# Kernel tuning notes

Hardware: AMD Instinct MI355X
Metric: run time of the kernel (lower is better)

The kernel has to match this reference:

```python
import jax, jax.numpy as jnp
import numpy as np

Q_MAX = 127.0  # int8 symmetric quant range
EPS = 1e-7

def setup_inputs() -> dict:
    key = jax.random.key(0)
    k1, k2, k3, k4 = jax.random.split(key, 4)
    M, K, N = 8192, 4096, 4096
    x = jax.random.normal(k1, (M, K), dtype=jnp.float32)
    # int8 weight stored as int32 for portability; values in [-127, 127]
    weight_i8 = jax.random.randint(k2, (N, K), -127, 128, dtype=jnp.int32)
    # per-output-channel weight scale (small positive)
    w_scale = jax.random.uniform(k3, (N,), dtype=jnp.float32) * 0.01 + 1e-4
    bias = jax.random.normal(k4, (N,), dtype=jnp.float32)
    return {"x": x, "weight_i8": weight_i8, "w_scale": w_scale, "bias": bias}

def reference(x, weight_i8, w_scale, bias):
    # per-token dynamic symmetric quantization of activations
    absmax = jnp.max(jnp.abs(x), axis=-1, keepdims=True)            # [M, 1]
    x_scale = jnp.maximum(absmax, EPS) / Q_MAX                       # [M, 1]
    x_q = jnp.clip(jnp.round(x / x_scale), -Q_MAX, Q_MAX)            # [M, K] int values in fp32
    acc = jnp.einsum('mk,nk->mn', x_q, weight_i8.astype(jnp.float32))  # [M, N]
    out = acc * x_scale * w_scale[None, :] + bias[None, :]
    return out
```

## Files before the change

### kernel.cpp

```cpp
#include <hip/hip_runtime.h>
#include <stdint.h>

#define Q_MAX_F 127.0f
#define EPS_F 1e-7f

typedef int   v4i  __attribute__((ext_vector_type(4)));
typedef int   v16i __attribute__((ext_vector_type(16)));
typedef float v4f  __attribute__((ext_vector_type(4)));

__global__ __launch_bounds__(256) void prep_kernel(
    const float* __restrict__ x, int8_t* __restrict__ xq,
    float* __restrict__ xscale,
    const int* __restrict__ w, int8_t* __restrict__ wq,
    int M, int K, long n4, int QB) {
  const int t = threadIdx.x;
  if ((int)blockIdx.x < QB) {
    __shared__ float sm[4];
    for (int row = blockIdx.x; row < M; row += QB) {
      const float* xr = x + (size_t)row * K + t * 16;
      float v[16];
      float m = 0.f;
#pragma unroll
      for (int c = 0; c < 4; ++c) {
        v4f f = *(const v4f*)(xr + c * 4);
#pragma unroll
        for (int j = 0; j < 4; ++j) {
          v[c * 4 + j] = f[j];
          m = fmaxf(m, fabsf(f[j]));
        }
      }
#pragma unroll
      for (int off = 32; off; off >>= 1) m = fmaxf(m, __shfl_xor(m, off));
      if ((t & 63) == 0) sm[t >> 6] = m;
      __syncthreads();
      m = fmaxf(fmaxf(sm[0], sm[1]), fmaxf(sm[2], sm[3]));
      __syncthreads();
      const float s = fmaxf(m, EPS_F) / Q_MAX_F;
      const float inv = 1.0f / s;
      if (t == 0) xscale[row] = s;
      v4i pk;
#pragma unroll
      for (int c = 0; c < 4; ++c) {
        int pw = 0;
#pragma unroll
        for (int j = 0; j < 4; ++j) {
          float q = rintf(v[c * 4 + j] * inv);
          q = fminf(fmaxf(q, -127.f), 127.f);
          pw |= ((int)q & 0xff) << (8 * j);
        }
        pk[c] = pw;
      }
      *(v4i*)(xq + (size_t)row * K + t * 16) = pk;
    }
  } else {
    const long stride = (long)(gridDim.x - QB) * 256;
    for (long i = (long)((int)blockIdx.x - QB) * 256 + t; i < n4; i += stride) {
      v4i a = ((const v4i*)w)[i];
      ((int*)wq)[i] = (a[0] & 0xff) | ((a[1] & 0xff) << 8) |
                      ((a[2] & 0xff) << 16) | ((a[3] & 0xff) << 24);
    }
  }
}

#define BM 256
#define BN 256

__global__ __launch_bounds__(512, 2) void w8a8_gemm_kernel(
    const int8_t* __restrict__ xq, const int8_t* __restrict__ wq,
    const float* __restrict__ xscale, const float* __restrict__ wscale,
    const float* __restrict__ bias, float* __restrict__ out,
    int M, int N, int K) {
  extern __shared__ char lds[];

  const int t = threadIdx.x;
  const int lane = t & 63;
  const int wid = t >> 6;
  const int wr = wid >> 2;
  const int wc = wid & 3;

  const int nwg = gridDim.x;
  int bid = blockIdx.x;
  int wg = ((nwg & 7) == 0) ? ((bid & 7) * (nwg >> 3) + (bid >> 3)) : bid;

  const int nbn = N / BN;
  const int bm = (wg / nbn) * BM;
  const int bn = (wg % nbn) * BN;

  const char* gA = (const char*)xq + (size_t)bm * K;
  const char* gB = (const char*)wq + (size_t)bn * K;

  v16i acc[4][2] = {};

  auto stage_part = [&](int kt, int p) {
    const char* gsrc = p ? gB : gA;
    char* dstbase = lds + (size_t)(kt & 3) * 32768 + p * 16384;
#pragma unroll
    for (int i = 0; i < 2; ++i) {
      const int lin = i * 8192 + wid * 1024 + lane * 16;
      const int row = lin >> 6;
      const int cs = (lane & 3) ^ ((row >> 1) & 3);
      const char* src = gsrc + (size_t)row * K + kt * 64 + cs * 16;
      __builtin_amdgcn_global_load_lds(
          (const __attribute__((address_space(1))) void*)src,
          (__attribute__((address_space(3))) void*)(dstbase + i * 8192 + wid * 1024),
          16, 0, 0);
    }
  };

  const int NT = K / 64;
  const int cl = lane & 31;
  const int ch = lane >> 5;

  for (int kt = 0; kt < 3; ++kt) { stage_part(kt, 0); stage_part(kt, 1); }
  asm volatile("s_waitcnt vmcnt(8)" ::: "memory");
  asm volatile("s_barrier" ::: "memory");

  for (int kt = 0; kt < NT; ++kt) {
    const char* bufA = lds + (size_t)(kt & 3) * 32768;
    const char* bufB = bufA + 16384;

    if (kt + 3 < NT) { stage_part(kt + 3, 0); stage_part(kt + 3, 1); }

    v4i a[2][4], b[2][2];
#pragma unroll
    for (int ks = 0; ks < 2; ++ks) {
#pragma unroll
      for (int fi = 0; fi < 4; ++fi) {
        const int r = wr * 128 + fi * 32 + cl;
        const int c = (ch + 2 * ks) ^ ((r >> 1) & 3);
        a[ks][fi] = *(const v4i*)(bufA + r * 64 + (c << 4));
      }
#pragma unroll
      for (int fj = 0; fj < 2; ++fj) {
        const int r = wc * 64 + fj * 32 + cl;
        const int c = (ch + 2 * ks) ^ ((r >> 1) & 3);
        b[ks][fj] = *(const v4i*)(bufB + r * 64 + (c << 4));
      }
    }

    __builtin_amdgcn_s_setprio(1);
#pragma unroll
    for (int ks = 0; ks < 2; ++ks)
#pragma unroll
      for (int fi = 0; fi < 4; ++fi)
#pragma unroll
        for (int fj = 0; fj < 2; ++fj)
          acc[fi][fj] = __builtin_amdgcn_mfma_i32_32x32x32_i8(
              a[ks][fi], b[ks][fj], acc[fi][fj], 0, 0, 0);
    __builtin_amdgcn_s_setprio(0);

    if (kt <= NT - 4)      asm volatile("s_waitcnt vmcnt(8)" ::: "memory");
    else if (kt == NT - 3) asm volatile("s_waitcnt vmcnt(4)" ::: "memory");
    else if (kt == NT - 2) asm volatile("s_waitcnt vmcnt(0)" ::: "memory");
    asm volatile("s_barrier" ::: "memory");
  }

  const int hl = lane >> 5;
  const float wsc0 = wscale[bn + wc * 64 + cl];
  const float wsc1 = wscale[bn + wc * 64 + 32 + cl];
  const float bs0 = bias[bn + wc * 64 + cl];
  const float bs1 = bias[bn + wc * 64 + 32 + cl];
#pragma unroll
  for (int fi = 0; fi < 4; ++fi) {
#pragma unroll
    for (int r = 0; r < 16; ++r) {
      const int grow = bm + wr * 128 + fi * 32 + (r & 3) + 8 * (r >> 2) + 4 * hl;
      const float xs = xscale[grow];
      float* orow = out + (size_t)grow * N + bn + wc * 64 + cl;
      orow[0]  = (float)acc[fi][0][r] * (xs * wsc0) + bs0;
      orow[32] = (float)acc[fi][1][r] * (xs * wsc1) + bs1;
    }
  }
}

extern "C" void kernel_launch(void* const* d_in, const int* in_sizes, int n_in,
                              void* d_out, int out_size, void* d_ws, size_t ws_size,
                              hipStream_t stream) {
  const float* x = (const float*)d_in[0];
  const int* w = (const int*)d_in[1];
  const float* wscale = (const float*)d_in[2];
  const float* bias = (const float*)d_in[3];
  float* out = (float*)d_out;

  const int N = in_sizes[2];
  const long wk = (long)in_sizes[1];
  const int K = (int)(wk / N);
  const int M = (int)((long)in_sizes[0] / K);

  int8_t* xq = (int8_t*)d_ws;
  int8_t* wq = xq + (size_t)M * K;
  float* xscale = (float*)(wq + (size_t)N * K);

  const long n4 = (long)N * K / 4;
  const int QB = 2048, PB = 2048;
  prep_kernel<<<QB + PB, 256, 0, stream>>>(x, xq, xscale, w, wq, M, K, n4, QB);

  const int nwg = (M / BM) * (N / BN);
  w8a8_gemm_kernel<<<nwg, 512, 131072, stream>>>(xq, wq, xscale, wscale, bias,
                                                 out, M, N, K);
}
```

Measured before the change: 415.2 us.

## Pre-pack operands in MFMA fragment order and load A directly to registers

The quantize and weight-pack kernels now write int8 data in a fragment-major layout that matches the MFMA operand order, so each lane's 16-byte fragment sits contiguous in global memory. The GEMM now loads A fragments straight from global into double-buffered registers, one tile ahead, and stages only B through LDS. This cuts the LDS footprint from 128KB of dynamic to 64KB of static and removes A's LDS traffic and swizzle math. In exchange, A's global loads are exposed to latency with only one stage of prefetch, and prep is split into two separate launches.

Result: slower. 458.2 us (+10.4%).

```diff
diff --git a/kernel.cpp b/kernel.cpp
--- a/kernel.cpp
+++ b/kernel.cpp
@@ -8,69 +8,91 @@
 typedef int   v16i __attribute__((ext_vector_type(16)));
 typedef float v4f  __attribute__((ext_vector_type(4)));
 
-__global__ __launch_bounds__(256) void prep_kernel(
+
+__global__ __launch_bounds__(256) void quant_x_kernel(
     const float* __restrict__ x, int8_t* __restrict__ xq,
-    float* __restrict__ xscale,
-    const int* __restrict__ w, int8_t* __restrict__ wq,
-    int M, int K, long n4, int QB) {
+    float* __restrict__ xscale, int M, int K, int QB) {
   const int t = threadIdx.x;
-  if ((int)blockIdx.x < QB) {
-    __shared__ float sm[4];
-    for (int row = blockIdx.x; row < M; row += QB) {
-      const float* xr = x + (size_t)row * K + t * 16;
-      float v[16];
-      float m = 0.f;
-#pragma unroll
-      for (int c = 0; c < 4; ++c) {
-        v4f f = *(const v4f*)(xr + c * 4);
-#pragma unroll
-        for (int j = 0; j < 4; ++j) {
-          v[c * 4 + j] = f[j];
-          m = fmaxf(m, fabsf(f[j]));
-        }
+  const int KT = K >> 6;
+  __shared__ float sm[4];
+  for (int row = blockIdx.x; row < M; row += QB) {
+    const float* xr = x + (size_t)row * K + t * 16;
+    float v[16];
+    float m = 0.f;
+#pragma unroll
+    for (int c = 0; c < 4; ++c) {
+      v4f f = *(const v4f*)(xr + c * 4);
+#pragma unroll
+      for (int j = 0; j < 4; ++j) {
+        v[c * 4 + j] = f[j];
+        m = fmaxf(m, fabsf(f[j]));
       }
-#pragma unroll
-      for (int off = 32; off; off >>= 1) m = fmaxf(m, __shfl_xor(m, off));
-      if ((t & 63) == 0) sm[t >> 6] = m;
-      __syncthreads();
-      m = fmaxf(fmaxf(sm[0], sm[1]), fmaxf(sm[2], sm[3]));
-      __syncthreads();
-      const float s = fmaxf(m, EPS_F) / Q_MAX_F;
-      const float inv = 1.0f / s;
-      if (t == 0) xscale[row] = s;
-      v4i pk;
-#pragma unroll
-      for (int c = 0; c < 4; ++c) {
-        int pw = 0;
-#pragma unroll
-        for (int j = 0; j < 4; ++j) {
-          float q = rintf(v[c * 4 + j] * inv);
-          q = fminf(fmaxf(q, -127.f), 127.f);
-          pw |= ((int)q & 0xff) << (8 * j);
-        }
-        pk[c] = pw;
+    }
+#pragma unroll
+    for (int off = 32; off; off >>= 1) m = fmaxf(m, __shfl_xor(m, off));
+    if ((t & 63) == 0) sm[t >> 6] = m;
+    __syncthreads();
+    m = fmaxf(fmaxf(sm[0], sm[1]), fmaxf(sm[2], sm[3]));
+    __syncthreads();
+    const float s = fmaxf(m, EPS_F) / Q_MAX_F;
+    const float inv = 1.0f / s;
+    if (t == 0) xscale[row] = s;
+    v4i pk;
+#pragma unroll
+    for (int c = 0; c < 4; ++c) {
+      int pw = 0;
+#pragma unroll
+      for (int j = 0; j < 4; ++j) {
+        float q = rintf(v[c * 4 + j] * inv);
+        q = fminf(fmaxf(q, -127.f), 127.f);
+        pw |= ((int)q & 0xff) << (8 * j);
       }
-      *(v4i*)(xq + (size_t)row * K + t * 16) = pk;
-    }
-  } else {
-    const long stride = (long)(gridDim.x - QB) * 256;
-    for (long i = (long)((int)blockIdx.x - QB) * 256 + t; i < n4; i += stride) {
-      v4i a = ((const v4i*)w)[i];
-      ((int*)wq)[i] = (a[0] & 0xff) | ((a[1] & 0xff) << 8) |
-                      ((a[2] & 0xff) << 16) | ((a[3] & 0xff) << 24);
-    }
-  }
-}
-
-#define BM 256
-#define BN 256
+      pk[c] = pw;
+    }
+    const int rb = row >> 7, f2 = (row >> 5) & 3, cl = row & 31;
+    const int kt = t >> 2, ks = (t >> 1) & 1, ch = t & 1;
+    const size_t flat =
+        ((((size_t)rb * KT + kt) * 2 + ks) * 4 + f2) * 64 + ch * 32 + cl;
+    *(v4i*)(xq + flat * 16) = pk;
+  }
+}
+
+__global__ __launch_bounds__(256) void pack_w_kernel(
+    const int* __restrict__ w, int8_t* __restrict__ wq, int K, long nchunks) {
+  const int KT = K >> 6;
+  const long stride = (long)gridDim.x * 256;
+  for (long o = (long)blockIdx.x * 256 + threadIdx.x; o < nchunks;
+       o += stride) {
+    const int cl = (int)(o & 31);
+    const int ch = (int)((o >> 5) & 1);
+    const int fj = (int)((o >> 6) & 1);
+    const int ks = (int)((o >> 7) & 1);
+    const long rest = o >> 8;
+    const int kt = (int)(rest & (KT - 1));
+    const long cb = rest >> 6;
+    const long n = cb * 64 + fj * 32 + cl;
+    const long k16 = (long)kt * 4 + ks * 2 + ch;
+    const int* src = w + n * K + k16 * 16;
+    v4i outw;
+#pragma unroll
+    for (int c = 0; c < 4; ++c) {
+      v4i a = *(const v4i*)(src + c * 4);
+      outw[c] = (a[0] & 0xff) | ((a[1] & 0xff) << 8) |
+                ((a[2] & 0xff) << 16) | ((a[3] & 0xff) << 24);
+    }
+    *(v4i*)(wq + o * 16) = outw;
+  }
+}
+
+#define BMg 256
+#define BNg 256
 
 __global__ __launch_bounds__(512, 2) void w8a8_gemm_kernel(
     const int8_t* __restrict__ xq, const int8_t* __restrict__ wq,
     const float* __restrict__ xscale, const float* __restrict__ wscale,
     const float* __restrict__ bias, float* __restrict__ out,
     int M, int N, int K) {
-  extern __shared__ char lds[];
+  __shared__ __align__(16) char lds[65536];
 
   const int t = threadIdx.x;
   const int lane = t & 63;
@@ -82,62 +104,53 @@
   int bid = blockIdx.x;
   int wg = ((nwg & 7) == 0) ? ((bid & 7) * (nwg >> 3) + (bid >> 3)) : bid;
 
-  const int nbn = N / BN;
-  const int bm = (wg / nbn) * BM;
-  const int bn = (wg % nbn) * BN;
-
-  const char* gA = (const char*)xq + (size_t)bm * K;
-  const char* gB = (const char*)wq + (size_t)bn * K;
+  const int nbn = N / BNg;
+  const int bm = (wg / nbn) * BMg;
+  const int bn = (wg % nbn) * BNg;
+
+  const int KT = K >> 6;
+  const int NT = KT;
+
+  const char* aBase = (const char*)xq +
+                      ((size_t)((bm >> 7) + wr) * KT) * 8192 +
+                      (size_t)lane * 16;
+  const char* bBase = (const char*)wq + ((size_t)(bn >> 6) * KT) * 4096;
 
   v16i acc[4][2] = {};
-
-  auto stage_part = [&](int kt, int p) {
-    const char* gsrc = p ? gB : gA;
-    char* dstbase = lds + (size_t)(kt & 3) * 32768 + p * 16384;
+  v4i aA[2][4], aB[2][4];
+
+  auto loadA = [&](v4i (*dst)[4], int kt) {
+    const char* p = aBase + (size_t)kt * 8192;
+#pragma unroll
+    for (int ks = 0; ks < 2; ++ks)
+#pragma unroll
+      for (int fi = 0; fi < 4; ++fi)
+        dst[ks][fi] = *(const v4i*)(p + (ks * 4 + fi) * 1024);
+  };
+  auto stageB = [&](int kt) {
 #pragma unroll
     for (int i = 0; i < 2; ++i) {
-      const int lin = i * 8192 + wid * 1024 + lane * 16;
-      const int row = lin >> 6;
-      const int cs = (lane & 3) ^ ((row >> 1) & 3);
-      const char* src = gsrc + (size_t)row * K + kt * 64 + cs * 16;
+      const int q = wid * 2 + i;
+      const char* src = bBase + ((size_t)(q >> 2) * KT + kt) * 4096 +
+                        (q & 3) * 1024 + (size_t)lane * 16;
       __builtin_amdgcn_global_load_lds(
           (const __attribute__((address_space(1))) void*)src,
-          (__attribute__((address_space(3))) void*)(dstbase + i * 8192 + wid * 1024),
+          (__attribute__((address_space(3))) void*)(lds + (kt & 3) * 16384 +
+                                                    q * 1024),
           16, 0, 0);
     }
   };
 
-  const int NT = K / 64;
-  const int cl = lane & 31;
-  const int ch = lane >> 5;
-
-  for (int kt = 0; kt < 3; ++kt) { stage_part(kt, 0); stage_part(kt, 1); }
-  asm volatile("s_waitcnt vmcnt(8)" ::: "memory");
-  asm volatile("s_barrier" ::: "memory");
-
-  for (int kt = 0; kt < NT; ++kt) {
-    const char* bufA = lds + (size_t)(kt & 3) * 32768;
-    const char* bufB = bufA + 16384;
-
-    if (kt + 3 < NT) { stage_part(kt + 3, 0); stage_part(kt + 3, 1); }
-
-    v4i a[2][4], b[2][2];
-#pragma unroll
-    for (int ks = 0; ks < 2; ++ks) {
-#pragma unroll
-      for (int fi = 0; fi < 4; ++fi) {
-        const int r = wr * 128 + fi * 32 + cl;
-        const int c = (ch + 2 * ks) ^ ((r >> 1) & 3);
-        a[ks][fi] = *(const v4i*)(bufA + r * 64 + (c << 4));
-      }
-#pragma unroll
-      for (int fj = 0; fj < 2; ++fj) {
-        const int r = wc * 64 + fj * 32 + cl;
-        const int c = (ch + 2 * ks) ^ ((r >> 1) & 3);
-        b[ks][fj] = *(const v4i*)(bufB + r * 64 + (c << 4));
-      }
-    }
-
+  auto body = [&](int kt, v4i (*cur)[4], v4i (*nxt)[4]) {
+    if (kt + 1 < NT) loadA(nxt, kt + 1);
+    if (kt + 3 < NT) stageB(kt + 3);
+    const char* slot = lds + (kt & 3) * 16384 + wc * 4096 + (size_t)lane * 16;
+    v4i bfr[2][2];
+#pragma unroll
+    for (int ks = 0; ks < 2; ++ks)
+#pragma unroll
+      for (int fj = 0; fj < 2; ++fj)
+        bfr[ks][fj] = *(const v4i*)(slot + (ks * 2 + fj) * 1024);
     __builtin_amdgcn_s_setprio(1);
 #pragma unroll
     for (int ks = 0; ks < 2; ++ks)
@@ -146,15 +159,26 @@
 #pragma unroll
         for (int fj = 0; fj < 2; ++fj)
           acc[fi][fj] = __builtin_amdgcn_mfma_i32_32x32x32_i8(
-              a[ks][fi], b[ks][fj], acc[fi][fj], 0, 0, 0);
+              cur[ks][fi], bfr[ks][fj], acc[fi][fj], 0, 0, 0);
     __builtin_amdgcn_s_setprio(0);
-
-    if (kt <= NT - 4)      asm volatile("s_waitcnt vmcnt(8)" ::: "memory");
-    else if (kt == NT - 3) asm volatile("s_waitcnt vmcnt(4)" ::: "memory");
-    else if (kt == NT - 2) asm volatile("s_waitcnt vmcnt(0)" ::: "memory");
-    asm volatile("s_barrier" ::: "memory");
-  }
-
+    if (kt + 1 < NT) {
+      if (kt + 3 < NT) asm volatile("s_waitcnt vmcnt(2)" ::: "memory");
+      else             asm volatile("s_waitcnt vmcnt(0)" ::: "memory");
+      asm volatile("s_barrier" ::: "memory");
+    }
+  };
+
+  loadA(aA, 0);
+  stageB(0); stageB(1); stageB(2);
+  asm volatile("s_waitcnt vmcnt(4)" ::: "memory");
+  asm volatile("s_barrier" ::: "memory");
+
+  for (int kt = 0; kt < NT; kt += 2) {
+    body(kt, aA, aB);
+    body(kt + 1, aB, aA);
+  }
+
+  const int cl = lane & 31;
   const int hl = lane >> 5;
   const float wsc0 = wscale[bn + wc * 64 + cl];
   const float wsc1 = wscale[bn + wc * 64 + 32 + cl];
@@ -191,11 +215,13 @@
   int8_t* wq = xq + (size_t)M * K;
   float* xscale = (float*)(wq + (size_t)N * K);
 
-  const long n4 = (long)N * K / 4;
-  const int QB = 2048, PB = 2048;
-  prep_kernel<<<QB + PB, 256, 0, stream>>>(x, xq, xscale, w, wq, M, K, n4, QB);
-
-  const int nwg = (M / BM) * (N / BN);
-  w8a8_gemm_kernel<<<nwg, 512, 131072, stream>>>(xq, wq, xscale, wscale, bias,
-                                                 out, M, N, K);
-}
+  const int QB = 2048;
+  quant_x_kernel<<<QB, 256, 0, stream>>>(x, xq, xscale, M, K, QB);
+
+  const long nchunks = (long)N * K / 16;
+  pack_w_kernel<<<2048, 256, 0, stream>>>(w, wq, K, nchunks);
+
+  const int nwg = (M / BMg) * (N / BNg);
+  w8a8_gemm_kernel<<<nwg, 512, 0, stream>>>(xq, wq, xscale, wscale, bias,
+                                            out, M, N, K);
+}
```
